# Kernel optimization log

Hardware: AMD Instinct MI355X
Metric: run time of the kernel (lower is better)

The kernel has to match this reference:

```python
import jax, jax.numpy as jnp
from jax import lax
import numpy as np

N_FFT = 1024
HOP = 256
CUTOFF = N_FFT // 2 + 1  # 513


def _make_bases():
    n = np.arange(N_FFT)
    # periodic hann window (scipy get_window('hann', N, fftbins=True))
    win = 0.5 - 0.5 * np.cos(2.0 * np.pi * n / N_FFT)
    fb = np.fft.fft(np.eye(N_FFT))
    FB = np.vstack([fb[:CUTOFF].real, fb[:CUTOFF].imag])  # [1026, 1024]
    scale = N_FFT / HOP
    fwd = (FB * win[None, :]).astype(np.float32)                      # [1026, 1024]
    inv = (np.linalg.pinv(scale * FB).T * win[None, :]).astype(np.float32)  # [1026, 1024]
    win_sq = (win ** 2).astype(np.float32)
    return jnp.asarray(fwd), jnp.asarray(inv), jnp.asarray(win_sq)

FWD_BASIS, INV_BASIS, WIN_SQ = _make_bases()


def setup_inputs() -> dict:
    key = jax.random.key(0)
    k1, k2 = jax.random.split(key)
    audio = jax.random.normal(k1, (4, 1048576), dtype=jnp.float32)
    bias_spec = jax.random.uniform(k2, (1, CUTOFF, 1), dtype=jnp.float32)
    return {"audio": audio, "bias_spec": bias_spec}


def reference(audio, bias_spec):
    strength = 0.1
    pad = N_FFT // 2
    # ---- STFT.transform: reflect pad + strided conv1d with fourier basis ----
    x = jnp.pad(audio, ((0, 0), (pad, pad)), mode='reflect')[:, None, :]  # [B,1,T+N]
    ft = lax.conv_general_dilated(
        x, FWD_BASIS[:, None, :], window_strides=(HOP,), padding='VALID',
        dimension_numbers=('NCH', 'OIH', 'NCH'))  # [B, 1026, F]
    re, im = ft[:, :CUTOFF, :], ft[:, CUTOFF:, :]
    mag = jnp.sqrt(re * re + im * im)
    phase = jnp.arctan2(im, re)
    # ---- denoise: bias subtract + clamp ----
    mag_d = jnp.maximum(mag - bias_spec * strength, 0.0)
    # ---- STFT.inverse: cos/sin recombine + conv_transpose1d ----
    rec = jnp.concatenate([mag_d * jnp.cos(phase), mag_d * jnp.sin(phase)], axis=1)  # [B,1026,F]
    # conv_transpose1d(stride=HOP) == dilated conv with flipped, channel-swapped kernel
    K = jnp.flip(INV_BASIS, axis=-1)[None, :, :]  # OIH: [1, 1026, 1024]
    inv = lax.conv_general_dilated(
        rec, K, window_strides=(1,), padding=[(N_FFT - 1, N_FFT - 1)],
        lhs_dilation=(HOP,), dimension_numbers=('NCH', 'OIH', 'NCH'))  # [B,1,(F-1)*HOP+N]
    # ---- window_sumsquare (vectorized overlap-add of win_sq) ----
    F = mag.shape[-1]
    n_len = N_FFT + HOP * (F - 1)
    idx = (jnp.arange(F)[:, None] * HOP + jnp.arange(N_FFT)[None, :]).reshape(-1)
    ws = jnp.zeros((n_len,), jnp.float32).at[idx].add(jnp.tile(WIN_SQ, F))
    tiny = jnp.finfo(jnp.float32).tiny
    inv = jnp.where(ws > tiny, inv / ws, inv) * (float(N_FFT) / HOP)
    # trim filter_length/2 from both ends
    return inv[:, :, pad:-pad]
```

## Files before the change

kernel.cpp:

```cpp
#include <hip/hip_runtime.h>
#include <math.h>


#define NFFT 1024
#define HOP  256
#define CUT  513
#define NB   4
#define LAUD 1048576
#define NFR  4097
#define NFRP 4224
#define FTROWS 4232
#define ABLEN 1082368

typedef __attribute__((ext_vector_type(4))) float f32x4;
typedef __attribute__((ext_vector_type(8))) short bf16x8;

__device__ __forceinline__ unsigned short f2bf(float x) {
    unsigned u = __float_as_uint(x);
    u += 0x7FFF + ((u >> 16) & 1);
    return (unsigned short)(u >> 16);
}

__global__ void build_bases_k(ushort* __restrict__ fwd, ushort* __restrict__ invW) {
    int idx = blockIdx.x * blockDim.x + threadIdx.x;
    if (idx >= 1024 * 1024) return;
    int c = idx >> 10, n = idx & 1023;
    const float CST = 6.135923151542565e-3f;
    float win = 0.5f - 0.5f * cosf(CST * (float)n);
    int k = (c < CUT) ? c : (c - 512);
    int m = (k * n) & 1023;
    float si, co;
    sincosf(CST * (float)m, &si, &co);
    float base = (c < CUT) ? co : -si;
    fwd[idx] = f2bf(base * win);
    float d = (c == 0 || c == 512) ? (1.0f / 1024.0f) : (2.0f / 1024.0f);
    invW[((n & 255) << 12) + ((n >> 8) << 10) + c] = f2bf(0.25f * base * d * win);
}

__global__ void cvt_audio_k(const float* __restrict__ audio, ushort* __restrict__ aud) {
    int idx = blockIdx.x * blockDim.x + threadIdx.x;
    if (idx >= NB * ABLEN) return;
    int t = idx % ABLEN;
    int b = idx / ABLEN;
    float v = 0.f;
    if (t < LAUD + 1024) {
        int j = t - 512;
        if (j < 0) j = -j;
        if (j >= LAUD) j = 2 * LAUD - 2 - j;
        v = audio[(long)b * LAUD + j];
    }
    aud[idx] = f2bf(v);
}

__global__ void zero_row_k(ushort* __restrict__ ft) {
    int idx = blockIdx.x * blockDim.x + threadIdx.x;
    if (idx >= NB * 1024) return;
    int b = idx >> 10, c = idx & 1023;
    ft[(long)b * FTROWS * 1024 + c] = 0;
}

__global__ __launch_bounds__(256) void gemm_fwd_k(
    const ushort* __restrict__ fwd, const ushort* __restrict__ aud,
    const float* __restrict__ bias, ushort* __restrict__ ft) {
    __shared__ char smem[32768];
    const int tid = threadIdx.x;
    const int wid = tid >> 6, lane = tid & 63;
    const int lh = lane & 15, lg = lane >> 4;
    const int wm = wid >> 1, wn = wid & 1;
    int w = (blockIdx.x & 7) * 132 + (blockIdx.x >> 3);
    const int f0 = (w % 33) << 7;
    const int c0 = ((w / 33) & 7) << 6;
    const int b  = w / 264;
    const ushort* ab = aud + (long)b * ABLEN;
    f32x4 acc[4][4] = {};

    for (int k0 = 0; k0 < 1024; k0 += 64) {
        if (k0) __syncthreads();
        #pragma unroll
        for (int i = 0; i < 4; ++i) {
            int ci = (i << 8) + tid;
            int row = ci >> 3;
            int ks = k0 + (((ci & 7) ^ (row & 7)) << 3);
            int grow = ((row >> 4) & 1) * 512 + c0 + ((row >> 5) << 4) + (row & 15);
            __builtin_amdgcn_global_load_lds(
                (const __attribute__((address_space(1))) unsigned int*)(fwd + (grow << 10) + ks),
                (__attribute__((address_space(3))) unsigned int*)(smem + (i << 12) + (wid << 10)),
                16, 0, 0);
            __builtin_amdgcn_global_load_lds(
                (const __attribute__((address_space(1))) unsigned int*)(ab + (f0 + row) * HOP + ks),
                (__attribute__((address_space(3))) unsigned int*)(smem + 16384 + (i << 12) + (wid << 10)),
                16, 0, 0);
        }
        __syncthreads();
        #pragma unroll
        for (int s = 0; s < 2; ++s) {
            bf16x8 av[4], bv[4];
            #pragma unroll
            for (int i = 0; i < 4; ++i) {
                int r = (wm << 6) + (i << 4) + lh;
                av[i] = *(const bf16x8*)(smem + (r << 7) + ((((s << 2) + lg) ^ (r & 7)) << 4));
                int q = (wn << 6) + (i << 4) + lh;
                bv[i] = *(const bf16x8*)(smem + 16384 + (q << 7) + ((((s << 2) + lg) ^ (q & 7)) << 4));
            }
            #pragma unroll
            for (int i = 0; i < 4; ++i)
                #pragma unroll
                for (int j = 0; j < 4; ++j)
                    acc[i][j] = __builtin_amdgcn_mfma_f32_16x16x32_bf16(av[i], bv[j], acc[i][j], 0, 0, 0);
        }
    }
    ushort* ftb = ft + (long)b * FTROWS * 1024 + 1024;
    float b512 = bias[512] * 0.1f;
    #pragma unroll
    for (int p = 0; p < 2; ++p) {
        int kbase = c0 + ((wm * 2 + p) << 4) + (lg << 2);
        float bs[4];
        #pragma unroll
        for (int q = 0; q < 4; ++q) bs[q] = bias[kbase + q] * 0.1f;
        #pragma unroll
        for (int j = 0; j < 4; ++j) {
            int f = f0 + (wn << 6) + (j << 4) + lh;
            bool valid = (f < NFR);
            ushort4 ore, oim;
            #pragma unroll
            for (int q = 0; q < 4; ++q) {
                float re = acc[2 * p][j][q], im = acc[2 * p + 1][j][q];
                float sre, sim;
                if (kbase + q == 0) {
                    float mre = fabsf(re), mim = fabsf(im);
                    sre = mre > 0.f ? fmaxf(mre - bs[0], 0.f) / mre : 0.f;
                    sim = mim > 0.f ? fmaxf(mim - b512, 0.f) / mim : 0.f;
                } else {
                    float mag = sqrtf(re * re + im * im);
                    float s = mag > 0.f ? fmaxf(mag - bs[q], 0.f) / mag : 0.f;
                    sre = s; sim = s;
                }
                float vre = valid ? re * sre : 0.f;
                float vim = valid ? im * sim : 0.f;
                ((unsigned short*)&ore)[q] = f2bf(vre);
                ((unsigned short*)&oim)[q] = f2bf(vim);
            }
            *(ushort4*)(ftb + ((long)f << 10) + kbase) = ore;
            *(ushort4*)(ftb + ((long)f << 10) + 512 + kbase) = oim;
        }
    }
}

__global__ __launch_bounds__(512) void gemm_ola_k(
    const ushort* __restrict__ invW, const ushort* __restrict__ ft,
    float* __restrict__ out) {
    __shared__ char smem[49152];
    const int tid = threadIdx.x;
    const int wid = tid >> 6, lane = tid & 63;
    const int lh = lane & 15, lg = lane >> 4;
    const int g = wid >> 2;
    const int wid2 = wid & 3;
    const int wm = wid2 >> 1, wn = wid2 & 1;
    const int tg = tid & 255;
    int w = (blockIdx.x & 7) * 64 + (blockIdx.x >> 3);
    const int h0  = (w & 1) << 7;
    const int fo0 = 2 + (((w >> 1) & 63) << 6);
    const int b   = w >> 7;
    const ushort* ftb = ft + (long)b * FTROWS * 1024;
    char* sm = smem + g * 24576;
    f32x4 acc[4][2] = {};

    for (int k0 = 0; k0 < 2048; k0 += 64) {
        if (k0) __syncthreads();
        int kk = (g << 11) + k0;
        int d  = kk >> 10;
        int cb = kk & 1023;
        #pragma unroll
        for (int i = 0; i < 4; ++i) {
            int ci = (i << 8) + tg;
            int row = ci >> 3;
            int swz = (((ci & 7) ^ (row & 7)) << 3);
            __builtin_amdgcn_global_load_lds(
                (const __attribute__((address_space(1))) unsigned int*)(invW + ((h0 + row) << 12) + kk + swz),
                (__attribute__((address_space(3))) unsigned int*)(sm + (i << 12) + (wid2 << 10)),
                16, 0, 0);
        }
        #pragma unroll
        for (int i = 0; i < 2; ++i) {
            int ci = (i << 8) + tg;
            int row = ci >> 3;
            int swz = (((ci & 7) ^ (row & 7)) << 3);
            int frow = fo0 + row - d + 1;
            __builtin_amdgcn_global_load_lds(
                (const __attribute__((address_space(1))) unsigned int*)(ftb + ((long)frow << 10) + cb + swz),
                (__attribute__((address_space(3))) unsigned int*)(sm + 16384 + (i << 12) + (wid2 << 10)),
                16, 0, 0);
        }
        __syncthreads();
        #pragma unroll
        for (int s = 0; s < 2; ++s) {
            bf16x8 av[4], bv[2];
            #pragma unroll
            for (int i = 0; i < 4; ++i) {
                int r = (wm << 6) + (i << 4) + lh;
                av[i] = *(const bf16x8*)(sm + (r << 7) + ((((s << 2) + lg) ^ (r & 7)) << 4));
            }
            #pragma unroll
            for (int j = 0; j < 2; ++j) {
                int rq = (wn << 5) + (j << 4) + lh;
                bv[j] = *(const bf16x8*)(sm + 16384 + (rq << 7) + ((((s << 2) + lg) ^ (rq & 7)) << 4));
            }
            #pragma unroll
            for (int i = 0; i < 4; ++i)
                #pragma unroll
                for (int j = 0; j < 2; ++j)
                    acc[i][j] = __builtin_amdgcn_mfma_f32_16x16x32_bf16(av[i], bv[j], acc[i][j], 0, 0, 0);
        }
    }
    __syncthreads();
    float* red = (float*)smem;
    if (g == 1) {
        #pragma unroll
        for (int i = 0; i < 4; ++i)
            #pragma unroll
            for (int j = 0; j < 2; ++j) {
                int hl = (wm << 6) + (i << 4) + (lg << 2);
                int fl = (wn << 5) + (j << 4) + lh;
                #pragma unroll
                for (int q = 0; q < 4; ++q)
                    red[(hl + q) * 64 + fl] = acc[i][j][q];
            }
    }
    __syncthreads();
    if (g == 1) return;
    float* ob = out + (long)b * LAUD;
    const float CST = 6.135923151542565e-3f;
    #pragma unroll
    for (int i = 0; i < 4; ++i) {
        int hbase = h0 + (wm << 6) + (i << 4) + (lg << 2);
        int hl = (wm << 6) + (i << 4) + (lg << 2);
        #pragma unroll
        for (int j = 0; j < 2; ++j) {
            int fo = fo0 + (wn << 5) + (j << 4) + lh;
            int fl = (wn << 5) + (j << 4) + lh;
            f32x4 v = acc[i][j];
            #pragma unroll
            for (int q = 0; q < 4; ++q) v[q] += red[(hl + q) * 64 + fl];
            if (fo == 2 || fo == 4097) {
                #pragma unroll
                for (int q = 0; q < 4; ++q) {
                    int n = (fo == 2) ? (hbase + q + 768) : (hbase + q);
                    float w2 = 0.5f - 0.5f * cosf(CST * (float)n);
                    v[q] = v[q] * (4.0f / (1.5f - w2 * w2));
                }
            } else {
                v *= (8.0f / 3.0f);
            }
            *(f32x4*)(ob + (((long)(fo - 2)) << 8) + hbase) = v;
        }
    }
}

extern "C" void kernel_launch(void* const* d_in, const int* in_sizes, int n_in,
                              void* d_out, int out_size, void* d_ws, size_t ws_size,
                              hipStream_t stream) {
    const float* audio = (const float*)d_in[0];
    const float* bias  = (const float*)d_in[1];
    float* out = (float*)d_out;
    char* wsb = (char*)d_ws;

    ushort* fwd  = (ushort*)(wsb);
    ushort* invW = (ushort*)(wsb + 2097152);
    ushort* aud  = (ushort*)(wsb + 4194304);
    ushort* ft   = (ushort*)(wsb + 12853248);

    build_bases_k<<<4096, 256, 0, stream>>>(fwd, invW);
    cvt_audio_k<<<(NB * ABLEN + 255) / 256, 256, 0, stream>>>(audio, aud);
    zero_row_k<<<(NB * 1024 + 255) / 256, 256, 0, stream>>>(ft);

    gemm_fwd_k<<<1056, 256, 0, stream>>>(fwd, aud, bias, ft);

    gemm_ola_k<<<512, 512, 0, stream>>>(invW, ft, out);
}
```

Before: 115.7 us.

## Double-buffer GEMM B tiles, load A directly to registers, fuse prep kernels

Both GEMM kernels now double-buffer the streamed B operand in LDS, prefetching the next k-tile while the current one is computed. The basis A operand is read straight from global memory into registers instead of being staged through LDS, which halves LDS use. The basis build uses a shared cosine table instead of per-element sincos. Audio conversion is vectorized to 8 elements per thread and absorbs the zero-row kernel, removing one launch. The trade-off is that direct global A loads rely on cache hits and may add latency on every k step.

After: 235.9 us. 2.04x slower.

```diff
diff --git a/kernel.cpp b/kernel.cpp
--- a/kernel.cpp
+++ b/kernel.cpp
@@ -15,48 +15,91 @@
 typedef __attribute__((ext_vector_type(4))) float f32x4;
 typedef __attribute__((ext_vector_type(8))) short bf16x8;
 
+#define AS1 __attribute__((address_space(1)))
+#define AS3 __attribute__((address_space(3)))
+
 __device__ __forceinline__ unsigned short f2bf(float x) {
     unsigned u = __float_as_uint(x);
     u += 0x7FFF + ((u >> 16) & 1);
     return (unsigned short)(u >> 16);
 }
 
-__global__ void build_bases_k(ushort* __restrict__ fwd, ushort* __restrict__ invW) {
+__global__ __launch_bounds__(256) void build_bases_k(
+    ushort* __restrict__ fwd, ushort* __restrict__ invW) {
+    __shared__ float ctab[1024];
+    const int tid = threadIdx.x, bx = blockIdx.x;
+    const float CST = 6.135923151542565e-3f;
+    #pragma unroll
+    for (int i = 0; i < 4; ++i) ctab[(i << 8) + tid] = cosf(CST * (float)((i << 8) + tid));
+    __syncthreads();
+    #pragma unroll
+    for (int r = 0; r < 4; ++r) {
+        int c = (bx << 2) + r;
+        int k = (c < CUT) ? c : (c - 512);
+        #pragma unroll
+        for (int ch = 0; ch < 4; ++ch) {
+            int n = (ch << 8) + tid;
+            int m = (k * n) & 1023;
+            float base = (c < CUT) ? ctab[m] : -ctab[(m + 768) & 1023];
+            float win = 0.5f - 0.5f * ctab[n];
+            fwd[(c << 10) + n] = f2bf(base * win);
+        }
+    }
+    #pragma unroll
+    for (int r = 0; r < 4; ++r) {
+        int n = (bx << 2) + r;
+        float win = 0.5f - 0.5f * ctab[n];
+        long obase = ((long)(n & 255) << 12) + ((long)(n >> 8) << 10);
+        #pragma unroll
+        for (int ch = 0; ch < 4; ++ch) {
+            int c = (ch << 8) + tid;
+            int k = (c < CUT) ? c : (c - 512);
+            int m = (k * n) & 1023;
+            float base = (c < CUT) ? ctab[m] : -ctab[(m + 768) & 1023];
+            float d = (c == 0 || c == 512) ? (1.0f / 1024.0f) : (2.0f / 1024.0f);
+            invW[obase + c] = f2bf(0.25f * base * d * win);
+        }
+    }
+}
+
+__global__ void cvt_audio_k(const float* __restrict__ audio,
+                            ushort* __restrict__ aud, ushort* __restrict__ ft) {
+    const int NV = ABLEN / 8;
     int idx = blockIdx.x * blockDim.x + threadIdx.x;
-    if (idx >= 1024 * 1024) return;
-    int c = idx >> 10, n = idx & 1023;
-    const float CST = 6.135923151542565e-3f;
-    float win = 0.5f - 0.5f * cosf(CST * (float)n);
-    int k = (c < CUT) ? c : (c - 512);
-    int m = (k * n) & 1023;
-    float si, co;
-    sincosf(CST * (float)m, &si, &co);
-    float base = (c < CUT) ? co : -si;
-    fwd[idx] = f2bf(base * win);
-    float d = (c == 0 || c == 512) ? (1.0f / 1024.0f) : (2.0f / 1024.0f);
-    invW[((n & 255) << 12) + ((n >> 8) << 10) + c] = f2bf(0.25f * base * d * win);
-}
-
-__global__ void cvt_audio_k(const float* __restrict__ audio, ushort* __restrict__ aud) {
-    int idx = blockIdx.x * blockDim.x + threadIdx.x;
-    if (idx >= NB * ABLEN) return;
-    int t = idx % ABLEN;
-    int b = idx / ABLEN;
-    float v = 0.f;
-    if (t < LAUD + 1024) {
-        int j = t - 512;
-        if (j < 0) j = -j;
-        if (j >= LAUD) j = 2 * LAUD - 2 - j;
-        v = audio[(long)b * LAUD + j];
-    }
-    aud[idx] = f2bf(v);
-}
-
-__global__ void zero_row_k(ushort* __restrict__ ft) {
-    int idx = blockIdx.x * blockDim.x + threadIdx.x;
-    if (idx >= NB * 1024) return;
-    int b = idx >> 10, c = idx & 1023;
-    ft[(long)b * FTROWS * 1024 + c] = 0;
+    if (idx < NB * NV) {
+        int b = idx / NV;
+        int t8 = (idx - b * NV) << 3;
+        const float* ap = audio + (long)b * LAUD;
+        ushort o[8];
+        int j0 = t8 - 512;
+        if (j0 >= 0 && j0 + 7 < LAUD) {
+            f32x4 v0 = *(const f32x4*)(ap + j0);
+            f32x4 v1 = *(const f32x4*)(ap + j0 + 4);
+            #pragma unroll
+            for (int q = 0; q < 4; ++q) { o[q] = f2bf(v0[q]); o[4 + q] = f2bf(v1[q]); }
+        } else {
+            #pragma unroll
+            for (int q = 0; q < 8; ++q) {
+                int t = t8 + q;
+                float v = 0.f;
+                if (t < LAUD + 1024) {
+                    int j = t - 512;
+                    if (j < 0) j = -j;
+                    if (j >= LAUD) j = 2 * LAUD - 2 - j;
+                    v = ap[j];
+                }
+                o[q] = f2bf(v);
+            }
+        }
+        *(ushort4*)(aud + (long)b * ABLEN + t8)     = *(ushort4*)&o[0];
+        *(ushort4*)(aud + (long)b * ABLEN + t8 + 4) = *(ushort4*)&o[4];
+    } else if (idx < NB * NV + 512) {
+        int e = idx - NB * NV;
+        int b = e >> 7, c8 = (e & 127) << 3;
+        ushort z[8] = {};
+        *(ushort4*)(ft + (long)b * FTROWS * 1024 + c8)     = *(ushort4*)&z[0];
+        *(ushort4*)(ft + (long)b * FTROWS * 1024 + c8 + 4) = *(ushort4*)&z[4];
+    }
 }
 
 __global__ __launch_bounds__(256) void gemm_fwd_k(
@@ -72,42 +115,63 @@
     const int c0 = ((w / 33) & 7) << 6;
     const int b  = w / 264;
     const ushort* ab = aud + (long)b * ABLEN;
+
+    const ushort* apt[4];
+    #pragma unroll
+    for (int i = 0; i < 4; ++i) {
+        int r = (wm << 6) + (i << 4) + lh;
+        int grow = ((r >> 4) & 1) * 512 + c0 + ((r >> 5) << 4) + (r & 15);
+        apt[i] = fwd + (grow << 10) + (lg << 3);
+    }
+
     f32x4 acc[4][4] = {};
+    #pragma unroll
+    for (int i = 0; i < 4; ++i) {
+        int ci = (i << 8) + tid;
+        int row = ci >> 3;
+        int ks = ((ci & 7) ^ (row & 7)) << 3;
+        __builtin_amdgcn_global_load_lds(
+            (const AS1 unsigned int*)(ab + (f0 + row) * HOP + ks),
+            (AS3 unsigned int*)(smem + (i << 12) + (wid << 10)), 16, 0, 0);
+    }
+    __syncthreads();
 
     for (int k0 = 0; k0 < 1024; k0 += 64) {
-        if (k0) __syncthreads();
+        const int cur = (k0 >> 6) & 1;
+        if (k0 < 960) {
+            #pragma unroll
+            for (int i = 0; i < 4; ++i) {
+                int ci = (i << 8) + tid;
+                int row = ci >> 3;
+                int ks = k0 + 64 + (((ci & 7) ^ (row & 7)) << 3);
+                __builtin_amdgcn_global_load_lds(
+                    (const AS1 unsigned int*)(ab + (f0 + row) * HOP + ks),
+                    (AS3 unsigned int*)(smem + ((cur ^ 1) << 14) + (i << 12) + (wid << 10)),
+                    16, 0, 0);
+            }
+        }
+        bf16x8 avA[4], avB[4];
         #pragma unroll
         for (int i = 0; i < 4; ++i) {
-            int ci = (i << 8) + tid;
-            int row = ci >> 3;
-            int ks = k0 + (((ci & 7) ^ (row & 7)) << 3);
-            int grow = ((row >> 4) & 1) * 512 + c0 + ((row >> 5) << 4) + (row & 15);
-            __builtin_amdgcn_global_load_lds(
-                (const __attribute__((address_space(1))) unsigned int*)(fwd + (grow << 10) + ks),
-                (__attribute__((address_space(3))) unsigned int*)(smem + (i << 12) + (wid << 10)),
-                16, 0, 0);
-            __builtin_amdgcn_global_load_lds(
-                (const __attribute__((address_space(1))) unsigned int*)(ab + (f0 + row) * HOP + ks),
-                (__attribute__((address_space(3))) unsigned int*)(smem + 16384 + (i << 12) + (wid << 10)),
-                16, 0, 0);
-        }
-        __syncthreads();
+            avA[i] = *(const bf16x8*)(apt[i] + k0);
+            avB[i] = *(const bf16x8*)(apt[i] + k0 + 32);
+        }
         #pragma unroll
         for (int s = 0; s < 2; ++s) {
-            bf16x8 av[4], bv[4];
+            bf16x8 bv[4];
             #pragma unroll
             for (int i = 0; i < 4; ++i) {
-                int r = (wm << 6) + (i << 4) + lh;
-                av[i] = *(const bf16x8*)(smem + (r << 7) + ((((s << 2) + lg) ^ (r & 7)) << 4));
                 int q = (wn << 6) + (i << 4) + lh;
-                bv[i] = *(const bf16x8*)(smem + 16384 + (q << 7) + ((((s << 2) + lg) ^ (q & 7)) << 4));
+                bv[i] = *(const bf16x8*)(smem + (cur << 14) + (q << 7) + ((((s << 2) + lg) ^ (q & 7)) << 4));
             }
             #pragma unroll
             for (int i = 0; i < 4; ++i)
                 #pragma unroll
                 for (int j = 0; j < 4; ++j)
-                    acc[i][j] = __builtin_amdgcn_mfma_f32_16x16x32_bf16(av[i], bv[j], acc[i][j], 0, 0, 0);
-        }
+                    acc[i][j] = __builtin_amdgcn_mfma_f32_16x16x32_bf16(
+                        s ? avB[i] : avA[i], bv[j], acc[i][j], 0, 0, 0);
+        }
+        __syncthreads();
     }
     ushort* ftb = ft + (long)b * FTROWS * 1024 + 1024;
     float b512 = bias[512] * 0.1f;
@@ -135,10 +199,8 @@
                     float s = mag > 0.f ? fmaxf(mag - bs[q], 0.f) / mag : 0.f;
                     sre = s; sim = s;
                 }
-                float vre = valid ? re * sre : 0.f;
-                float vim = valid ? im * sim : 0.f;
-                ((unsigned short*)&ore)[q] = f2bf(vre);
-                ((unsigned short*)&oim)[q] = f2bf(vim);
+                ((unsigned short*)&ore)[q] = f2bf(valid ? re * sre : 0.f);
+                ((unsigned short*)&oim)[q] = f2bf(valid ? im * sim : 0.f);
             }
             *(ushort4*)(ftb + ((long)f << 10) + kbase) = ore;
             *(ushort4*)(ftb + ((long)f << 10) + 512 + kbase) = oim;
@@ -149,7 +211,7 @@
 __global__ __launch_bounds__(512) void gemm_ola_k(
     const ushort* __restrict__ invW, const ushort* __restrict__ ft,
     float* __restrict__ out) {
-    __shared__ char smem[49152];
+    __shared__ char smem[32768];
     const int tid = threadIdx.x;
     const int wid = tid >> 6, lane = tid & 63;
     const int lh = lane & 15, lg = lane >> 4;
@@ -162,24 +224,19 @@
     const int fo0 = 2 + (((w >> 1) & 63) << 6);
     const int b   = w >> 7;
     const ushort* ftb = ft + (long)b * FTROWS * 1024;
-    char* sm = smem + g * 24576;
+    char* sg = smem + g * 16384;
+
+    const ushort* apt[4];
+    #pragma unroll
+    for (int i = 0; i < 4; ++i) {
+        int r = (wm << 6) + (i << 4) + lh;
+        apt[i] = invW + ((long)(h0 + r) << 12) + (g << 11) + (lg << 3);
+    }
+
     f32x4 acc[4][2] = {};
-
-    for (int k0 = 0; k0 < 2048; k0 += 64) {
-        if (k0) __syncthreads();
-        int kk = (g << 11) + k0;
-        int d  = kk >> 10;
-        int cb = kk & 1023;
-        #pragma unroll
-        for (int i = 0; i < 4; ++i) {
-            int ci = (i << 8) + tg;
-            int row = ci >> 3;
-            int swz = (((ci & 7) ^ (row & 7)) << 3);
-            __builtin_amdgcn_global_load_lds(
-                (const __attribute__((address_space(1))) unsigned int*)(invW + ((h0 + row) << 12) + kk + swz),
-                (__attribute__((address_space(3))) unsigned int*)(sm + (i << 12) + (wid2 << 10)),
-                16, 0, 0);
-        }
+    {
+        int kk = g << 11;
+        int d = kk >> 10, cb = kk & 1023;
         #pragma unroll
         for (int i = 0; i < 2; ++i) {
             int ci = (i << 8) + tg;
@@ -187,32 +244,52 @@
             int swz = (((ci & 7) ^ (row & 7)) << 3);
             int frow = fo0 + row - d + 1;
             __builtin_amdgcn_global_load_lds(
-                (const __attribute__((address_space(1))) unsigned int*)(ftb + ((long)frow << 10) + cb + swz),
-                (__attribute__((address_space(3))) unsigned int*)(sm + 16384 + (i << 12) + (wid2 << 10)),
-                16, 0, 0);
-        }
-        __syncthreads();
+                (const AS1 unsigned int*)(ftb + ((long)frow << 10) + cb + swz),
+                (AS3 unsigned int*)(sg + (i << 12) + (wid2 << 10)), 16, 0, 0);
+        }
+    }
+    __syncthreads();
+
+    for (int k0 = 0; k0 < 2048; k0 += 64) {
+        const int cur = (k0 >> 6) & 1;
+        if (k0 < 1984) {
+            int kk = (g << 11) + k0 + 64;
+            int d = kk >> 10, cb = kk & 1023;
+            #pragma unroll
+            for (int i = 0; i < 2; ++i) {
+                int ci = (i << 8) + tg;
+                int row = ci >> 3;
+                int swz = (((ci & 7) ^ (row & 7)) << 3);
+                int frow = fo0 + row - d + 1;
+                __builtin_amdgcn_global_load_lds(
+                    (const AS1 unsigned int*)(ftb + ((long)frow << 10) + cb + swz),
+                    (AS3 unsigned int*)(sg + ((cur ^ 1) << 13) + (i << 12) + (wid2 << 10)),
+                    16, 0, 0);
+            }
+        }
+        bf16x8 avA[4], avB[4];
+        #pragma unroll
+        for (int i = 0; i < 4; ++i) {
+            avA[i] = *(const bf16x8*)(apt[i] + k0);
+            avB[i] = *(const bf16x8*)(apt[i] + k0 + 32);
+        }
         #pragma unroll
         for (int s = 0; s < 2; ++s) {
-            bf16x8 av[4], bv[2];
-            #pragma unroll
-            for (int i = 0; i < 4; ++i) {
-                int r = (wm << 6) + (i << 4) + lh;
-                av[i] = *(const bf16x8*)(sm + (r << 7) + ((((s << 2) + lg) ^ (r & 7)) << 4));
-            }
+            bf16x8 bv[2];
             #pragma unroll
             for (int j = 0; j < 2; ++j) {
                 int rq = (wn << 5) + (j << 4) + lh;
-                bv[j] = *(const bf16x8*)(sm + 16384 + (rq << 7) + ((((s << 2) + lg) ^ (rq & 7)) << 4));
+                bv[j] = *(const bf16x8*)(sg + (cur << 13) + (rq << 7) + ((((s << 2) + lg) ^ (rq & 7)) << 4));
             }
             #pragma unroll
             for (int i = 0; i < 4; ++i)
                 #pragma unroll
                 for (int j = 0; j < 2; ++j)
-                    acc[i][j] = __builtin_amdgcn_mfma_f32_16x16x32_bf16(av[i], bv[j], acc[i][j], 0, 0, 0);
-        }
-    }
-    __syncthreads();
+                    acc[i][j] = __builtin_amdgcn_mfma_f32_16x16x32_bf16(
+                        s ? avB[i] : avA[i], bv[j], acc[i][j], 0, 0, 0);
+        }
+        __syncthreads();
+    }
     float* red = (float*)smem;
     if (g == 1) {
         #pragma unroll
@@ -269,9 +346,10 @@
     ushort* aud  = (ushort*)(wsb + 4194304);
     ushort* ft   = (ushort*)(wsb + 12853248);
 
-    build_bases_k<<<4096, 256, 0, stream>>>(fwd, invW);
-    cvt_audio_k<<<(NB * ABLEN + 255) / 256, 256, 0, stream>>>(audio, aud);
-    zero_row_k<<<(NB * 1024 + 255) / 256, 256, 0, stream>>>(ft);
+    build_bases_k<<<256, 256, 0, stream>>>(fwd, invW);
+
+    int cvt_total = NB * (ABLEN / 8) + 512;
+    cvt_audio_k<<<(cvt_total + 255) / 256, 256, 0, stream>>>(audio, aud, ft);
 
     gemm_fwd_k<<<1056, 256, 0, stream>>>(fwd, aud, bias, ft);
 
```
